# Kernel tuning notes

Hardware: AMD Instinct MI355X
Metric: run time of the kernel (lower is better)

The kernel has to match this reference:

```python
import jax, jax.numpy as jnp
import numpy as np

NUM_ROUNDS = 2
NUM_REVERSE_ROUNDS = 2


def _scatter_mean(x, src, dst, n):
    # PyG mean aggregation: out[i] = mean_{(src->i) in E} x[src]; 0 if no in-edges.
    deg = jax.ops.segment_sum(jnp.ones((src.shape[0],), x.dtype), dst, num_segments=n)
    s = jax.ops.segment_sum(x[src], dst, num_segments=n)
    return s / jnp.maximum(deg, 1.0)[:, None]


def setup_inputs() -> dict:
    key = jax.random.key(0)
    ks = jax.random.split(key, 12)
    N_TEXT, N_NON, E, EMB, R = 100000, 10000, 500000, 256, 500
    N = N_TEXT + N_NON
    PRED_IN = 4 * EMB + 2 * 2 + 2 * 2 * (NUM_ROUNDS + NUM_REVERSE_ROUNDS)  # 1044
    return {
        "h_id_tensor": jax.random.randint(ks[0], (E,), 0, N),
        "r_id_tensor": jax.random.randint(ks[1], (E,), 0, R),
        "t_id_tensor": jax.random.randint(ks[2], (E,), 0, N),
        "q_emb": jax.random.normal(ks[3], (EMB,), jnp.float32),
        "entity_embs": jax.random.normal(ks[4], (N_TEXT, EMB), jnp.float32),
        "num_non_text_entities": N_NON,
        "relation_embs": jax.random.normal(ks[5], (R, EMB), jnp.float32),
        "topic_entity_one_hot": jax.random.uniform(ks[6], (N, 2), jnp.float32),
        "non_text_emb": jax.random.normal(ks[7], (1, EMB), jnp.float32),
        "W1": jax.random.normal(ks[8], (PRED_IN, EMB), jnp.float32) * 0.02,
        "b1": jnp.zeros((EMB,), jnp.float32),
        "W2": jax.random.normal(ks[9], (EMB, 1), jnp.float32) * 0.02,
        "b2": jnp.zeros((1,), jnp.float32),
    }


def reference(h_id_tensor, r_id_tensor, t_id_tensor, q_emb, entity_embs,
              num_non_text_entities, relation_embs, topic_entity_one_hot,
              non_text_emb, W1, b1, W2, b2):
    n = entity_embs.shape[0] + num_non_text_entities
    # h_e base: text entity embs + broadcast non-text embedding
    h_e0 = jnp.concatenate(
        [entity_embs, jnp.broadcast_to(non_text_emb, (num_non_text_entities, non_text_emb.shape[1]))],
        axis=0)
    h_e_list = [h_e0, topic_entity_one_hot]
    # DDE forward rounds: messages flow h_id -> t_id
    h_pe = topic_entity_one_hot
    for _ in range(NUM_ROUNDS):
        h_pe = _scatter_mean(h_pe, h_id_tensor, t_id_tensor, n)
        h_e_list.append(h_pe)
    # reverse rounds: messages flow t_id -> h_id
    h_pe = topic_entity_one_hot
    for _ in range(NUM_REVERSE_ROUNDS):
        h_pe = _scatter_mean(h_pe, t_id_tensor, h_id_tensor, n)
        h_e_list.append(h_pe)
    h_e = jnp.concatenate(h_e_list, axis=1)  # [N, emb + 2 + 2*(R+Rr)]
    e = h_id_tensor.shape[0]
    h_triple = jnp.concatenate(
        [jnp.broadcast_to(q_emb[None, :], (e, q_emb.shape[0])),
         h_e[h_id_tensor],
         relation_embs[r_id_tensor],
         h_e[t_id_tensor]], axis=1)  # [E, 1044]
    hidden = jax.nn.relu(h_triple @ W1 + b1)
    return hidden @ W2 + b2
```

## Files before the change

kernel.cpp:

```cpp
#include <hip/hip_runtime.h>
#include <stdint.h>

#define EMB 256
#define LDKB 288
#define DDE 10

typedef __attribute__((ext_vector_type(8))) short short8;
typedef __attribute__((ext_vector_type(4))) float f32x4;

__device__ __forceinline__ unsigned short f2bf(float f) {
    union { float f; unsigned int u; } v; v.f = f;
    unsigned int u = v.u;
    unsigned int r = (u + 0x7FFFu + ((u >> 16) & 1u)) >> 16;
    return (unsigned short)r;
}
__device__ __forceinline__ float bf2f(unsigned short b) {
    union { unsigned int u; float f; } v; v.u = ((unsigned int)b) << 16;
    return v.f;
}

#define FPSCALE 1048576.0f
#define FPINV   (1.0f / 1048576.0f)

__device__ __forceinline__ unsigned long long pack2(float a, float b) {
    unsigned int ua = (unsigned int)(a * FPSCALE);
    unsigned int ub = (unsigned int)(b * FPSCALE);
    return ((unsigned long long)ua << 36) | ((unsigned long long)ub << 10);
}
__device__ __forceinline__ float2 unpack2(unsigned long long v) {
    float d = fmaxf((float)(unsigned int)(v & 0x3FFULL), 1.0f);
    return make_float2((float)((v >> 36) & 0x3FFFFFFULL) * FPINV / d,
                       (float)((v >> 10) & 0x3FFFFFFULL) * FPINV / d);
}
__device__ __forceinline__ float2 unpack2d(unsigned long long v, float d) {
    return make_float2((float)((v >> 36) & 0x3FFFFFFULL) * FPINV / d,
                       (float)((v >> 10) & 0x3FFFFFFULL) * FPINV / d);
}


__global__ void k_r1_fused(const int* __restrict__ h_id, const int* __restrict__ t_id,
                           const float2* __restrict__ topic,
                           unsigned long long* __restrict__ fwd,
                           unsigned long long* __restrict__ rev, int E, int SC1, int COPY, int WT_BLK,
                           int TOTAL,
                           const float4* __restrict__ entity, const float4* __restrict__ nontext,
                           ushort4* __restrict__ he4, int n_text, int N,
                           const float* __restrict__ W1, unsigned short* __restrict__ wT,
                           const float* __restrict__ qv, const float* __restrict__ rel,
                           const float* __restrict__ b1, unsigned short* __restrict__ Prb) {
    const int b = blockIdx.x;
    const int sc_before = (int)(((long long)b * SC1) / TOTAL);
    const int is_scatter = (int)(((long long)(b + 1) * SC1) / TOTAL) != sc_before;
    if (is_scatter) {
        int e = sc_before * 256 + threadIdx.x;
        if (e >= E) return;
        int h = h_id[e], t = t_id[e];
        float2 th = topic[h];
        float2 tt = topic[t];
        atomicAdd(&fwd[t], pack2(th.x, th.y) | 1ULL);
        atomicAdd(&rev[h], pack2(tt.x, tt.y) | 1ULL);
        return;
    }
    const int o = b - sc_before;
    if (o < COPY) {
        int idx = o * 256 + threadIdx.x;
        int n = idx >> 6, q = idx & 63;
        float4 v = make_float4(0.f, 0.f, 0.f, 0.f);
        if (n < N) v = (n < n_text) ? entity[(size_t)n * 64 + q] : nontext[q];
        he4[(size_t)n * 64 + q] = make_ushort4(f2bf(v.x), f2bf(v.y), f2bf(v.z), f2bf(v.w));
    } else if (o < COPY + WT_BLK) {
        int idx = (o - COPY) * 256 + threadIdx.x;
        int j = idx / LDKB;
        int k = idx - j * LDKB;
        int col   = (j < EMB) ? j : (j - EMB);
        int baseE = (j < EMB) ? 256 : 778;
        int baseD = (j < EMB) ? 512 : 1034;
        float v = 0.0f;
        if (k < EMB)            v = W1[(long long)(baseE + k) * EMB + col];
        else if (k < EMB + DDE) v = W1[(long long)(baseD + (k - EMB)) * EMB + col];
        wT[idx] = f2bf(v);
    } else {
        int r = o - COPY - WT_BLK;
        int j = threadIdx.x;
        float acc = b1[j];
        for (int k = 0; k < EMB; ++k)
            acc = fmaf(qv[k], W1[(long long)k * EMB + j], acc);
        const float* relr = rel + (long long)r * EMB;
        for (int k = 0; k < EMB; ++k)
            acc = fmaf(relr[k], W1[(long long)(522 + k) * EMB + j], acc);
        Prb[(long long)r * EMB + j] = f2bf(acc);
    }
}


__global__ void k_r2(const int* __restrict__ h_id, const int* __restrict__ t_id,
                     const unsigned long long* __restrict__ fwd,
                     const unsigned long long* __restrict__ rev,
                     unsigned long long* __restrict__ s2,
                     unsigned long long* __restrict__ sr2, int E) {
    int e = blockIdx.x * blockDim.x + threadIdx.x;
    if (e >= E) return;
    int h = h_id[e], t = t_id[e];
    float2 dh = unpack2(fwd[h]);
    float2 rt = unpack2(rev[t]);
    atomicAdd(&s2[t], pack2(dh.x, dh.y));
    atomicAdd(&sr2[h], pack2(rt.x, rt.y));
}

__global__ __launch_bounds__(512) void k_gemm(const unsigned short* __restrict__ he,
                                              const unsigned short* __restrict__ wT,
                                              unsigned short* __restrict__ Ph,
                                              unsigned short* __restrict__ Pt,
                                              const float2* __restrict__ topic,
                                              const unsigned long long* __restrict__ fwd,
                                              const unsigned long long* __restrict__ rev,
                                              const unsigned long long* __restrict__ s2,
                                              const unsigned long long* __restrict__ sr2,
                                              int N) {
    __shared__ __align__(16) unsigned short lA[2][128 * 32];
    __shared__ __align__(16) unsigned short lB[2][256 * 32];
    const int t = threadIdx.x;
    const int lane = t & 63;
    const int w = t >> 6;
    const int bswz = (blockIdx.x & 7) * ((int)gridDim.x >> 3) + (blockIdx.x >> 3);
    const int br = bswz >> 1;
    const int bc = bswz & 1;
    const int wr = w >> 2;
    const int wc = w & 3;

    f32x4 acc[4][4];
#pragma unroll
    for (int r = 0; r < 4; ++r)
#pragma unroll
        for (int c = 0; c < 4; ++c)
            acc[r][c] = (f32x4){0.f, 0.f, 0.f, 0.f};

    const char* baseA = (const char*)he + (size_t)(br * 128) * (EMB * 2);
    const char* baseB = (const char*)wT + (size_t)(bc * 256) * (LDKB * 2);

    const int rowX = t >> 2;
    const int colb = (t & 3) * 16;

    auto stage = [&](int k0, int buf) {
        if (k0 < EMB) {
            const char* srcA = baseA + (size_t)rowX * (EMB * 2) + k0 * 2 + colb;
            __builtin_amdgcn_global_load_lds((const __attribute__((address_space(1))) void*)srcA,
                                             (__attribute__((address_space(3))) void*)((char*)lA[buf] + t * 16), 16, 0, 0);
        } else {
            const int n = br * 128 + rowX;
            short8 hv = (short8){0, 0, 0, 0, 0, 0, 0, 0};
            const int q4 = t & 3;
            if (n < N) {
                if (q4 == 0) {
                    float2 tp = topic[n];
                    unsigned long long f = fwd[n];
                    unsigned long long r = rev[n];
                    float df = fmaxf((float)(unsigned int)(f & 0x3FFULL), 1.0f);
                    float2 d1 = unpack2d(f, df);
                    float2 d2 = unpack2d(s2[n], df);
                    float2 r1 = unpack2(r);
                    hv[0] = (short)f2bf(tp.x); hv[1] = (short)f2bf(tp.y);
                    hv[2] = (short)f2bf(d1.x); hv[3] = (short)f2bf(d1.y);
                    hv[4] = (short)f2bf(d2.x); hv[5] = (short)f2bf(d2.y);
                    hv[6] = (short)f2bf(r1.x); hv[7] = (short)f2bf(r1.y);
                } else if (q4 == 1) {
                    unsigned long long r = rev[n];
                    float dr = fmaxf((float)(unsigned int)(r & 0x3FFULL), 1.0f);
                    float2 r2 = unpack2d(sr2[n], dr);
                    hv[0] = (short)f2bf(r2.x); hv[1] = (short)f2bf(r2.y);
                }
            }
            *(short8*)((char*)lA[buf] + rowX * 64 + q4 * 16) = hv;
        }
        const char* srcB0 = baseB + (size_t)rowX * (LDKB * 2) + k0 * 2 + colb;
        const char* srcB1 = baseB + (size_t)(rowX + 128) * (LDKB * 2) + k0 * 2 + colb;
        __builtin_amdgcn_global_load_lds((const __attribute__((address_space(1))) void*)srcB0,
                                         (__attribute__((address_space(3))) void*)((char*)lB[buf] + t * 16), 16, 0, 0);
        __builtin_amdgcn_global_load_lds((const __attribute__((address_space(1))) void*)srcB1,
                                         (__attribute__((address_space(3))) void*)((char*)lB[buf] + 8192 + t * 16), 16, 0, 0);
    };

    const int NK = LDKB / 32;
    stage(0, 0);
    __syncthreads();

    for (int k = 0; k < NK; ++k) {
        const int cur = k & 1;
        if (k + 1 < NK) stage((k + 1) * 32, cur ^ 1);

        short8 af[4], bfr[4];
#pragma unroll
        for (int r = 0; r < 4; ++r) {
            int arow = wr * 64 + r * 16 + (lane & 15);
            af[r] = *(const short8*)(lA[cur] + arow * 32 + (lane >> 4) * 8);
        }
#pragma unroll
        for (int c = 0; c < 4; ++c) {
            int brow = wc * 64 + c * 16 + (lane & 15);
            bfr[c] = *(const short8*)(lB[cur] + brow * 32 + (lane >> 4) * 8);
        }
#pragma unroll
        for (int r = 0; r < 4; ++r)
#pragma unroll
            for (int c = 0; c < 4; ++c)
                acc[r][c] = __builtin_amdgcn_mfma_f32_16x16x32_bf16(af[r], bfr[c], acc[r][c], 0, 0, 0);

        __syncthreads();
    }

    unsigned short* Pout = bc ? Pt : Ph;
    const int nbase = wc * 64;
    const int mbase = br * 128 + wr * 64 + (lane >> 4) * 4;
#pragma unroll
    for (int r = 0; r < 4; ++r) {
#pragma unroll
        for (int c = 0; c < 4; ++c) {
            int n = nbase + c * 16 + (lane & 15);
#pragma unroll
            for (int i = 0; i < 4; ++i) {
                int m = mbase + r * 16 + i;
                Pout[(size_t)m * EMB + n] = f2bf(acc[r][c][i]);
            }
        }
    }
}

__global__ __launch_bounds__(256) void k_edge(
    const int* __restrict__ h_id, const int* __restrict__ r_id, const int* __restrict__ t_id,
    const unsigned short* __restrict__ Ph, const unsigned short* __restrict__ Pt,
    const unsigned short* __restrict__ Prb, const float* __restrict__ W2,
    const float* __restrict__ b2, float* __restrict__ out, int E) {
    int lane = threadIdx.x & 63;
    int gw = (blockIdx.x * blockDim.x + threadIdx.x) >> 6;
    int nw = (gridDim.x * blockDim.x) >> 6;
    float4 w2 = *(const float4*)(W2 + 4 * lane);
    float bb = b2[0];
    const int lo = 4 * lane;
    for (int e = gw; e < E; e += nw) {
        int h = h_id[e], r = r_id[e], t = t_id[e];
        ushort4 ph = *(const ushort4*)(Ph + (size_t)h * EMB + lo);
        ushort4 pt = *(const ushort4*)(Pt + (size_t)t * EMB + lo);
        ushort4 pr = *(const ushort4*)(Prb + (size_t)r * EMB + lo);
        float v, acc;
        v = bf2f(pr.x) + bf2f(ph.x) + bf2f(pt.x); acc  = fmaxf(v, 0.f) * w2.x;
        v = bf2f(pr.y) + bf2f(ph.y) + bf2f(pt.y); acc += fmaxf(v, 0.f) * w2.y;
        v = bf2f(pr.z) + bf2f(ph.z) + bf2f(pt.z); acc += fmaxf(v, 0.f) * w2.z;
        v = bf2f(pr.w) + bf2f(ph.w) + bf2f(pt.w); acc += fmaxf(v, 0.f) * w2.w;
#pragma unroll
        for (int m = 32; m >= 1; m >>= 1) acc += __shfl_xor(acc, m, 64);
        if (lane == 0) out[e] = acc + bb;
    }
}


extern "C" void kernel_launch(void* const* d_in, const int* in_sizes, int n_in,
                              void* d_out, int out_size, void* d_ws, size_t ws_size,
                              hipStream_t stream) {
    const int*   h_id    = (const int*)d_in[0];
    const int*   r_id    = (const int*)d_in[1];
    const int*   t_id    = (const int*)d_in[2];
    const float* q       = (const float*)d_in[3];
    const float* entity  = (const float*)d_in[4];
    const float* rel     = (const float*)d_in[6];
    const float* topic   = (const float*)d_in[7];
    const float* nontext = (const float*)d_in[8];
    const float* W1      = (const float*)d_in[9];
    const float* b1      = (const float*)d_in[10];
    const float* W2      = (const float*)d_in[11];
    const float* b2      = (const float*)d_in[12];

    const int E      = in_sizes[0];
    const int n_text = in_sizes[4] / EMB;
    const int N      = in_sizes[7] / 2;
    const int R      = in_sizes[6] / EMB;
    const int Mpad   = (N + 127) & ~127;

    char* p = (char*)d_ws;
    auto alloc = [&](size_t bytes) {
        char* r = p;
        p += (bytes + 255) & ~(size_t)255;
        return r;
    };
    unsigned long long* fwd = (unsigned long long*)alloc((size_t)Mpad * 8);
    unsigned long long* rev = (unsigned long long*)alloc((size_t)Mpad * 8);
    unsigned long long* s2  = (unsigned long long*)alloc((size_t)Mpad * 8);
    unsigned long long* sr2 = (unsigned long long*)alloc((size_t)Mpad * 8);
    size_t zero_bytes = (size_t)(p - (char*)d_ws);
    unsigned short* he  = (unsigned short*)alloc((size_t)Mpad * EMB * 2);
    unsigned short* wT  = (unsigned short*)alloc((size_t)512 * LDKB * 2);
    unsigned short* Prb = (unsigned short*)alloc((size_t)R * EMB * 2);
    unsigned short* Ph  = (unsigned short*)alloc((size_t)Mpad * EMB * 2);
    unsigned short* Pt  = (unsigned short*)alloc((size_t)Mpad * EMB * 2);

    hipMemsetAsync(d_ws, 0, zero_bytes, stream);

    const int T = 256;
    const int SC1 = (E + T - 1) / T;
    const int COPY = Mpad / 4;
    const int WT_BLK = (512 * LDKB) / T;
    const int TOTAL = SC1 + COPY + WT_BLK + R;

    k_r1_fused<<<TOTAL, T, 0, stream>>>(
        h_id, t_id, (const float2*)topic, fwd, rev, E, SC1, COPY, WT_BLK, TOTAL,
        (const float4*)entity, (const float4*)nontext, (ushort4*)he, n_text, N,
        W1, wT, q, rel, b1, Prb);
    k_r2<<<SC1, T, 0, stream>>>(h_id, t_id, fwd, rev, s2, sr2, E);

    k_gemm<<<(Mpad / 128) * 2, 512, 0, stream>>>(he, wT, Ph, Pt,
                                                 (const float2*)topic, fwd, rev, s2, sr2, N);

    k_edge<<<4096, T, 0, stream>>>(h_id, r_id, t_id, Ph, Pt, Prb, W2, b2, (float*)d_out, E);
}
```

Measured before the change: 296.2 us.

## Overlap second DDE scatter round with node GEMM by moving round-2 terms to edge kernel

The second-round scatter (s2/sr2) no longer runs as its own kernel before the GEMM. Its blocks are interleaved into the GEMM launch, and the GEMM A-tile now carries only the topic, round-1 and reverse round-1 features. The round-2 contributions are instead packed per node by a small k_pack kernel and applied in the edge kernel through a per-column coefficient table (cw) taken from W1. The aim is to drop a dependent launch and run atomics alongside the matrix work, at the cost of an extra pack kernel, an extra 8-byte gather per edge endpoint, and 16 more FMAs per lane per edge.

```diff
diff --git a/kernel.cpp b/kernel.cpp
--- a/kernel.cpp
+++ b/kernel.cpp
@@ -42,12 +42,13 @@
                            const float2* __restrict__ topic,
                            unsigned long long* __restrict__ fwd,
                            unsigned long long* __restrict__ rev, int E, int SC1, int COPY, int WT_BLK,
-                           int TOTAL,
+                           int R, int TOTAL,
                            const float4* __restrict__ entity, const float4* __restrict__ nontext,
                            ushort4* __restrict__ he4, int n_text, int N,
                            const float* __restrict__ W1, unsigned short* __restrict__ wT,
                            const float* __restrict__ qv, const float* __restrict__ rel,
-                           const float* __restrict__ b1, unsigned short* __restrict__ Prb) {
+                           const float* __restrict__ b1, unsigned short* __restrict__ Prb,
+                           float* __restrict__ cw) {
     const int b = blockIdx.x;
     const int sc_before = (int)(((long long)b * SC1) / TOTAL);
     const int is_scatter = (int)(((long long)(b + 1) * SC1) / TOTAL) != sc_before;
@@ -79,7 +80,7 @@
         if (k < EMB)            v = W1[(long long)(baseE + k) * EMB + col];
         else if (k < EMB + DDE) v = W1[(long long)(baseD + (k - EMB)) * EMB + col];
         wT[idx] = f2bf(v);
-    } else {
+    } else if (o < COPY + WT_BLK + R) {
         int r = o - COPY - WT_BLK;
         int j = threadIdx.x;
         float acc = b1[j];
@@ -89,40 +90,51 @@
         for (int k = 0; k < EMB; ++k)
             acc = fmaf(relr[k], W1[(long long)(522 + k) * EMB + j], acc);
         Prb[(long long)r * EMB + j] = f2bf(acc);
-    }
-}
-
-
-__global__ void k_r2(const int* __restrict__ h_id, const int* __restrict__ t_id,
-                     const unsigned long long* __restrict__ fwd,
-                     const unsigned long long* __restrict__ rev,
-                     unsigned long long* __restrict__ s2,
-                     unsigned long long* __restrict__ sr2, int E) {
-    int e = blockIdx.x * blockDim.x + threadIdx.x;
-    if (e >= E) return;
-    int h = h_id[e], t = t_id[e];
-    float2 dh = unpack2(fwd[h]);
-    float2 rt = unpack2(rev[t]);
-    atomicAdd(&s2[t], pack2(dh.x, dh.y));
-    atomicAdd(&sr2[h], pack2(rt.x, rt.y));
-}
-
-__global__ __launch_bounds__(512) void k_gemm(const unsigned short* __restrict__ he,
-                                              const unsigned short* __restrict__ wT,
-                                              unsigned short* __restrict__ Ph,
-                                              unsigned short* __restrict__ Pt,
-                                              const float2* __restrict__ topic,
-                                              const unsigned long long* __restrict__ fwd,
-                                              const unsigned long long* __restrict__ rev,
-                                              const unsigned long long* __restrict__ s2,
-                                              const unsigned long long* __restrict__ sr2,
-                                              int N) {
+    } else {
+        int idx = (o - COPY - WT_BLK - R) * 256 + threadIdx.x;
+        if (idx < 2048) {
+            int j = idx >> 2, c = idx & 3;
+            int col   = (j < EMB) ? j : (j - EMB);
+            int baseD = (j < EMB) ? 512 : 1034;
+            int row   = baseD + ((c < 2) ? (4 + c) : (8 + (c - 2)));
+            cw[idx] = W1[(long long)row * EMB + col];
+        }
+    }
+}
+
+__global__ __launch_bounds__(512) void k_gemm_r2(const unsigned short* __restrict__ he,
+                                                 const unsigned short* __restrict__ wT,
+                                                 unsigned short* __restrict__ Ph,
+                                                 unsigned short* __restrict__ Pt,
+                                                 const float2* __restrict__ topic,
+                                                 const unsigned long long* __restrict__ fwd,
+                                                 const unsigned long long* __restrict__ rev,
+                                                 unsigned long long* __restrict__ s2,
+                                                 unsigned long long* __restrict__ sr2,
+                                                 const int* __restrict__ h_id,
+                                                 const int* __restrict__ t_id,
+                                                 int N, int E, int GB, int TOTAL) {
     __shared__ __align__(16) unsigned short lA[2][128 * 32];
     __shared__ __align__(16) unsigned short lB[2][256 * 32];
+    const int b = blockIdx.x;
+    const int g_before = (int)(((long long)b * GB) / TOTAL);
+    const int is_gemm = (int)(((long long)(b + 1) * GB) / TOTAL) != g_before;
+    if (!is_gemm) {
+        int e = (b - g_before) * 512 + threadIdx.x;
+        if (e < E) {
+            int h = h_id[e], t = t_id[e];
+            float2 dh = unpack2(fwd[h]);
+            float2 rt = unpack2(rev[t]);
+            atomicAdd(&s2[t], pack2(dh.x, dh.y));
+            atomicAdd(&sr2[h], pack2(rt.x, rt.y));
+        }
+        return;
+    }
     const int t = threadIdx.x;
     const int lane = t & 63;
     const int w = t >> 6;
-    const int bswz = (blockIdx.x & 7) * ((int)gridDim.x >> 3) + (blockIdx.x >> 3);
+    const int o = g_before;
+    const int bswz = (o & 7) * (GB >> 3) + (o >> 3);
     const int br = bswz >> 1;
     const int bc = bswz & 1;
     const int wr = w >> 2;
@@ -150,25 +162,15 @@
             const int n = br * 128 + rowX;
             short8 hv = (short8){0, 0, 0, 0, 0, 0, 0, 0};
             const int q4 = t & 3;
-            if (n < N) {
-                if (q4 == 0) {
-                    float2 tp = topic[n];
-                    unsigned long long f = fwd[n];
-                    unsigned long long r = rev[n];
-                    float df = fmaxf((float)(unsigned int)(f & 0x3FFULL), 1.0f);
-                    float2 d1 = unpack2d(f, df);
-                    float2 d2 = unpack2d(s2[n], df);
-                    float2 r1 = unpack2(r);
-                    hv[0] = (short)f2bf(tp.x); hv[1] = (short)f2bf(tp.y);
-                    hv[2] = (short)f2bf(d1.x); hv[3] = (short)f2bf(d1.y);
-                    hv[4] = (short)f2bf(d2.x); hv[5] = (short)f2bf(d2.y);
-                    hv[6] = (short)f2bf(r1.x); hv[7] = (short)f2bf(r1.y);
-                } else if (q4 == 1) {
-                    unsigned long long r = rev[n];
-                    float dr = fmaxf((float)(unsigned int)(r & 0x3FFULL), 1.0f);
-                    float2 r2 = unpack2d(sr2[n], dr);
-                    hv[0] = (short)f2bf(r2.x); hv[1] = (short)f2bf(r2.y);
-                }
+            if (n < N && q4 == 0) {
+                float2 tp = topic[n];
+                unsigned long long f = fwd[n];
+                unsigned long long r = rev[n];
+                float2 d1 = unpack2(f);
+                float2 r1 = unpack2(r);
+                hv[0] = (short)f2bf(tp.x); hv[1] = (short)f2bf(tp.y);
+                hv[2] = (short)f2bf(d1.x); hv[3] = (short)f2bf(d1.y);
+                hv[6] = (short)f2bf(r1.x); hv[7] = (short)f2bf(r1.y);
             }
             *(short8*)((char*)lA[buf] + rowX * 64 + q4 * 16) = hv;
         }
@@ -225,27 +227,61 @@
     }
 }
 
+__global__ void k_pack(const unsigned long long* __restrict__ fwd,
+                       const unsigned long long* __restrict__ rev,
+                       const unsigned long long* __restrict__ s2,
+                       const unsigned long long* __restrict__ sr2,
+                       ushort4* __restrict__ dr2, int N, int Mpad) {
+    int n = blockIdx.x * blockDim.x + threadIdx.x;
+    if (n >= Mpad) return;
+    ushort4 v = make_ushort4(0, 0, 0, 0);
+    if (n < N) {
+        float df = fmaxf((float)(unsigned int)(fwd[n] & 0x3FFULL), 1.0f);
+        float dr = fmaxf((float)(unsigned int)(rev[n] & 0x3FFULL), 1.0f);
+        float2 d2 = unpack2d(s2[n], df);
+        float2 r2 = unpack2d(sr2[n], dr);
+        v = make_ushort4(f2bf(d2.x), f2bf(d2.y), f2bf(r2.x), f2bf(r2.y));
+    }
+    dr2[n] = v;
+}
+
 __global__ __launch_bounds__(256) void k_edge(
     const int* __restrict__ h_id, const int* __restrict__ r_id, const int* __restrict__ t_id,
     const unsigned short* __restrict__ Ph, const unsigned short* __restrict__ Pt,
-    const unsigned short* __restrict__ Prb, const float* __restrict__ W2,
+    const unsigned short* __restrict__ Prb, const ushort4* __restrict__ dr2,
+    const float4* __restrict__ cw, const float* __restrict__ W2,
     const float* __restrict__ b2, float* __restrict__ out, int E) {
     int lane = threadIdx.x & 63;
     int gw = (blockIdx.x * blockDim.x + threadIdx.x) >> 6;
     int nw = (gridDim.x * blockDim.x) >> 6;
-    float4 w2 = *(const float4*)(W2 + 4 * lane);
+    const int lo = 4 * lane;
+    float w2c[4];
+    *(float4*)w2c = *(const float4*)(W2 + lo);
     float bb = b2[0];
-    const int lo = 4 * lane;
+    float4 cH[4], cT[4];
+#pragma unroll
+    for (int c = 0; c < 4; ++c) { cH[c] = cw[lo + c]; cT[c] = cw[256 + lo + c]; }
+
     for (int e = gw; e < E; e += nw) {
         int h = h_id[e], r = r_id[e], t = t_id[e];
         ushort4 ph = *(const ushort4*)(Ph + (size_t)h * EMB + lo);
         ushort4 pt = *(const ushort4*)(Pt + (size_t)t * EMB + lo);
         ushort4 pr = *(const ushort4*)(Prb + (size_t)r * EMB + lo);
-        float v, acc;
-        v = bf2f(pr.x) + bf2f(ph.x) + bf2f(pt.x); acc  = fmaxf(v, 0.f) * w2.x;
-        v = bf2f(pr.y) + bf2f(ph.y) + bf2f(pt.y); acc += fmaxf(v, 0.f) * w2.y;
-        v = bf2f(pr.z) + bf2f(ph.z) + bf2f(pt.z); acc += fmaxf(v, 0.f) * w2.z;
-        v = bf2f(pr.w) + bf2f(ph.w) + bf2f(pt.w); acc += fmaxf(v, 0.f) * w2.w;
+        ushort4 dh = dr2[h];
+        ushort4 dt = dr2[t];
+        float d2hx = bf2f(dh.x), d2hy = bf2f(dh.y), r2hx = bf2f(dh.z), r2hy = bf2f(dh.w);
+        float d2tx = bf2f(dt.x), d2ty = bf2f(dt.y), r2tx = bf2f(dt.z), r2ty = bf2f(dt.w);
+        const unsigned short* phs = (const unsigned short*)&ph;
+        const unsigned short* pts = (const unsigned short*)&pt;
+        const unsigned short* prs = (const unsigned short*)&pr;
+        float acc = 0.f;
+#pragma unroll
+        for (int c = 0; c < 4; ++c) {
+            float v = bf2f(prs[c]) + bf2f(phs[c]) + bf2f(pts[c]);
+            v += d2hx * cH[c].x + d2hy * cH[c].y + r2hx * cH[c].z + r2hy * cH[c].w;
+            v += d2tx * cT[c].x + d2ty * cT[c].y + r2tx * cT[c].z + r2ty * cT[c].w;
+            acc += fmaxf(v, 0.f) * w2c[c];
+        }
 #pragma unroll
         for (int m = 32; m >= 1; m >>= 1) acc += __shfl_xor(acc, m, 64);
         if (lane == 0) out[e] = acc + bb;
@@ -291,6 +327,8 @@
     unsigned short* Prb = (unsigned short*)alloc((size_t)R * EMB * 2);
     unsigned short* Ph  = (unsigned short*)alloc((size_t)Mpad * EMB * 2);
     unsigned short* Pt  = (unsigned short*)alloc((size_t)Mpad * EMB * 2);
+    ushort4*        dr2 = (ushort4*)alloc((size_t)Mpad * 8);
+    float*          cw  = (float*)alloc((size_t)512 * 4 * 4);
 
     hipMemsetAsync(d_ws, 0, zero_bytes, stream);
 
@@ -298,16 +336,22 @@
     const int SC1 = (E + T - 1) / T;
     const int COPY = Mpad / 4;
     const int WT_BLK = (512 * LDKB) / T;
-    const int TOTAL = SC1 + COPY + WT_BLK + R;
-
-    k_r1_fused<<<TOTAL, T, 0, stream>>>(
-        h_id, t_id, (const float2*)topic, fwd, rev, E, SC1, COPY, WT_BLK, TOTAL,
+    const int COEF = 8;
+    const int TOTAL1 = SC1 + COPY + WT_BLK + R + COEF;
+
+    k_r1_fused<<<TOTAL1, T, 0, stream>>>(
+        h_id, t_id, (const float2*)topic, fwd, rev, E, SC1, COPY, WT_BLK, R, TOTAL1,
         (const float4*)entity, (const float4*)nontext, (ushort4*)he, n_text, N,
-        W1, wT, q, rel, b1, Prb);
-    k_r2<<<SC1, T, 0, stream>>>(h_id, t_id, fwd, rev, s2, sr2, E);
-
-    k_gemm<<<(Mpad / 128) * 2, 512, 0, stream>>>(he, wT, Ph, Pt,
-                                                 (const float2*)topic, fwd, rev, s2, sr2, N);
-
-    k_edge<<<4096, T, 0, stream>>>(h_id, r_id, t_id, Ph, Pt, Prb, W2, b2, (float*)d_out, E);
-}
+        W1, wT, q, rel, b1, Prb, cw);
+
+    const int GB  = (Mpad / 128) * 2;
+    const int R2B = (E + 511) / 512;
+    k_gemm_r2<<<GB + R2B, 512, 0, stream>>>(he, wT, Ph, Pt,
+                                            (const float2*)topic, fwd, rev, s2, sr2,
+                                            h_id, t_id, N, E, GB, GB + R2B);
+
+    k_pack<<<(Mpad + T - 1) / T, T, 0, stream>>>(fwd, rev, s2, sr2, dr2, N, Mpad);
+
+    k_edge<<<4096, T, 0, stream>>>(h_id, r_id, t_id, Ph, Pt, Prb, dr2,
+                                   (const float4*)cw, W2, b2, (float*)d_out, E);
+}
```

Result: no change. 294.1 us (-0.7%).

## Merge both scatter rounds into one kernel with a global completion flag

Applied to the files above, without the earlier changes.

Folds the second scatter-mean round into the first fused kernel. Round-2 blocks spin on a global counter until every round-1 scatter block has finished, and scatter and copy blocks are interleaved so independent copy work fills the gaps. This removes one kernel launch and its boundary, and lets the copy, weight-transpose and relation-projection work overlap with both scatter phases. The risk is a deadlock if the waiting blocks occupy all slots before the round-1 blocks are scheduled, which the code relies on dispatch order to avoid. It also adds spin-wait overhead and fences.

```diff
diff --git a/kernel.cpp b/kernel.cpp
--- a/kernel.cpp
+++ b/kernel.cpp
@@ -38,73 +38,100 @@
 }
 
 
-__global__ void k_r1_fused(const int* __restrict__ h_id, const int* __restrict__ t_id,
-                           const float2* __restrict__ topic,
-                           unsigned long long* __restrict__ fwd,
-                           unsigned long long* __restrict__ rev, int E, int SC1, int COPY, int WT_BLK,
-                           int TOTAL,
-                           const float4* __restrict__ entity, const float4* __restrict__ nontext,
-                           ushort4* __restrict__ he4, int n_text, int N,
-                           const float* __restrict__ W1, unsigned short* __restrict__ wT,
-                           const float* __restrict__ qv, const float* __restrict__ rel,
-                           const float* __restrict__ b1, unsigned short* __restrict__ Prb) {
+__global__ __launch_bounds__(256, 8) void k_mega(
+    const int* __restrict__ h_id, const int* __restrict__ t_id,
+    const float2* __restrict__ topic,
+    unsigned long long* __restrict__ fwd, unsigned long long* __restrict__ rev,
+    unsigned long long* __restrict__ s2, unsigned long long* __restrict__ sr2,
+    unsigned long long* __restrict__ flag,
+    int E, int SC1, int R2B, int COPY_C, int WT_BLK,
+    const float4* __restrict__ entity, const float4* __restrict__ nontext,
+    ushort4* __restrict__ he4, int n_text, int N,
+    const float* __restrict__ W1, unsigned short* __restrict__ wT,
+    const float* __restrict__ qv, const float* __restrict__ rel,
+    const float* __restrict__ b1, unsigned short* __restrict__ Prb) {
     const int b = blockIdx.x;
-    const int sc_before = (int)(((long long)b * SC1) / TOTAL);
-    const int is_scatter = (int)(((long long)(b + 1) * SC1) / TOTAL) != sc_before;
-    if (is_scatter) {
-        int e = sc_before * 256 + threadIdx.x;
-        if (e >= E) return;
-        int h = h_id[e], t = t_id[e];
-        float2 th = topic[h];
-        float2 tt = topic[t];
-        atomicAdd(&fwd[t], pack2(th.x, th.y) | 1ULL);
-        atomicAdd(&rev[h], pack2(tt.x, tt.y) | 1ULL);
-        return;
+    const int A = 2 * SC1, B = 2 * R2B;
+    int copyIdx;
+    if (b < A) {
+        if (!(b & 1)) {
+            int e = (b >> 1) * 256 + threadIdx.x;
+            if (e < E) {
+                int h = h_id[e], t = t_id[e];
+                float2 th = topic[h];
+                float2 tt = topic[t];
+                unsigned long long o1 = atomicAdd(&fwd[t], pack2(th.x, th.y) | 1ULL);
+                unsigned long long o2 = atomicAdd(&rev[h], pack2(tt.x, tt.y) | 1ULL);
+                asm volatile("" :: "v"(o1), "v"(o2));
+            }
+            __threadfence();
+            __syncthreads();
+            if (threadIdx.x == 0) atomicAdd(flag, 1ULL);
+            return;
+        }
+        copyIdx = b >> 1;
+    } else if (b < A + B) {
+        const int q = b - A;
+        if (!(q & 1)) {
+            const int blk = q >> 1;
+            if (threadIdx.x == 0) {
+                while (__hip_atomic_load(flag, __ATOMIC_ACQUIRE, __HIP_MEMORY_SCOPE_AGENT)
+                       < (unsigned long long)SC1)
+                    __builtin_amdgcn_s_sleep(16);
+            }
+            __syncthreads();
+#pragma unroll
+            for (int it = 0; it < 2; ++it) {
+                int e = blk * 512 + it * 256 + threadIdx.x;
+                if (e < E) {
+                    int h = h_id[e], t = t_id[e];
+                    unsigned long long f = __hip_atomic_load(&fwd[h], __ATOMIC_RELAXED,
+                                                             __HIP_MEMORY_SCOPE_AGENT);
+                    unsigned long long r = __hip_atomic_load(&rev[t], __ATOMIC_RELAXED,
+                                                             __HIP_MEMORY_SCOPE_AGENT);
+                    float2 dh = unpack2(f);
+                    float2 rt = unpack2(r);
+                    atomicAdd(&s2[t], pack2(dh.x, dh.y));
+                    atomicAdd(&sr2[h], pack2(rt.x, rt.y));
+                }
+            }
+            return;
+        }
+        copyIdx = SC1 + (q >> 1);
+    } else {
+        const int q = b - A - B;
+        if (q < COPY_C) {
+            copyIdx = SC1 + R2B + q;
+        } else if (q < COPY_C + WT_BLK) {
+            int idx = (q - COPY_C) * 256 + threadIdx.x;
+            int j = idx / LDKB;
+            int k = idx - j * LDKB;
+            int col   = (j < EMB) ? j : (j - EMB);
+            int baseE = (j < EMB) ? 256 : 778;
+            int baseD = (j < EMB) ? 512 : 1034;
+            float v = 0.0f;
+            if (k < EMB)            v = W1[(long long)(baseE + k) * EMB + col];
+            else if (k < EMB + DDE) v = W1[(long long)(baseD + (k - EMB)) * EMB + col];
+            wT[idx] = f2bf(v);
+            return;
+        } else {
+            int r = q - COPY_C - WT_BLK;
+            int j = threadIdx.x;
+            float acc = b1[j];
+            for (int k = 0; k < EMB; ++k)
+                acc = fmaf(qv[k], W1[(long long)k * EMB + j], acc);
+            const float* relr = rel + (long long)r * EMB;
+            for (int k = 0; k < EMB; ++k)
+                acc = fmaf(relr[k], W1[(long long)(522 + k) * EMB + j], acc);
+            Prb[(long long)r * EMB + j] = f2bf(acc);
+            return;
+        }
     }
-    const int o = b - sc_before;
-    if (o < COPY) {
-        int idx = o * 256 + threadIdx.x;
-        int n = idx >> 6, q = idx & 63;
-        float4 v = make_float4(0.f, 0.f, 0.f, 0.f);
-        if (n < N) v = (n < n_text) ? entity[(size_t)n * 64 + q] : nontext[q];
-        he4[(size_t)n * 64 + q] = make_ushort4(f2bf(v.x), f2bf(v.y), f2bf(v.z), f2bf(v.w));
-    } else if (o < COPY + WT_BLK) {
-        int idx = (o - COPY) * 256 + threadIdx.x;
-        int j = idx / LDKB;
-        int k = idx - j * LDKB;
-        int col   = (j < EMB) ? j : (j - EMB);
-        int baseE = (j < EMB) ? 256 : 778;
-        int baseD = (j < EMB) ? 512 : 1034;
-        float v = 0.0f;
-        if (k < EMB)            v = W1[(long long)(baseE + k) * EMB + col];
-        else if (k < EMB + DDE) v = W1[(long long)(baseD + (k - EMB)) * EMB + col];
-        wT[idx] = f2bf(v);
-    } else {
-        int r = o - COPY - WT_BLK;
-        int j = threadIdx.x;
-        float acc = b1[j];
-        for (int k = 0; k < EMB; ++k)
-            acc = fmaf(qv[k], W1[(long long)k * EMB + j], acc);
-        const float* relr = rel + (long long)r * EMB;
-        for (int k = 0; k < EMB; ++k)
-            acc = fmaf(relr[k], W1[(long long)(522 + k) * EMB + j], acc);
-        Prb[(long long)r * EMB + j] = f2bf(acc);
-    }
-}
-
-
-__global__ void k_r2(const int* __restrict__ h_id, const int* __restrict__ t_id,
-                     const unsigned long long* __restrict__ fwd,
-                     const unsigned long long* __restrict__ rev,
-                     unsigned long long* __restrict__ s2,
-                     unsigned long long* __restrict__ sr2, int E) {
-    int e = blockIdx.x * blockDim.x + threadIdx.x;
-    if (e >= E) return;
-    int h = h_id[e], t = t_id[e];
-    float2 dh = unpack2(fwd[h]);
-    float2 rt = unpack2(rev[t]);
-    atomicAdd(&s2[t], pack2(dh.x, dh.y));
-    atomicAdd(&sr2[h], pack2(rt.x, rt.y));
+    int idx = copyIdx * 256 + threadIdx.x;
+    int n = idx >> 6, qq = idx & 63;
+    float4 v = make_float4(0.f, 0.f, 0.f, 0.f);
+    if (n < N) v = (n < n_text) ? entity[(size_t)n * 64 + qq] : nontext[qq];
+    he4[(size_t)n * 64 + qq] = make_ushort4(f2bf(v.x), f2bf(v.y), f2bf(v.z), f2bf(v.w));
 }
 
 __global__ __launch_bounds__(512) void k_gemm(const unsigned short* __restrict__ he,
@@ -281,10 +308,11 @@
         p += (bytes + 255) & ~(size_t)255;
         return r;
     };
-    unsigned long long* fwd = (unsigned long long*)alloc((size_t)Mpad * 8);
-    unsigned long long* rev = (unsigned long long*)alloc((size_t)Mpad * 8);
-    unsigned long long* s2  = (unsigned long long*)alloc((size_t)Mpad * 8);
-    unsigned long long* sr2 = (unsigned long long*)alloc((size_t)Mpad * 8);
+    unsigned long long* fwd  = (unsigned long long*)alloc((size_t)Mpad * 8);
+    unsigned long long* rev  = (unsigned long long*)alloc((size_t)Mpad * 8);
+    unsigned long long* s2   = (unsigned long long*)alloc((size_t)Mpad * 8);
+    unsigned long long* sr2  = (unsigned long long*)alloc((size_t)Mpad * 8);
+    unsigned long long* flag = (unsigned long long*)alloc(256);
     size_t zero_bytes = (size_t)(p - (char*)d_ws);
     unsigned short* he  = (unsigned short*)alloc((size_t)Mpad * EMB * 2);
     unsigned short* wT  = (unsigned short*)alloc((size_t)512 * LDKB * 2);
@@ -295,16 +323,18 @@
     hipMemsetAsync(d_ws, 0, zero_bytes, stream);
 
     const int T = 256;
-    const int SC1 = (E + T - 1) / T;
-    const int COPY = Mpad / 4;
+    const int SC1    = (E + T - 1) / T;
+    const int R2B    = (E + 511) / 512;
+    const int COPY   = Mpad / 4;
+    const int COPY_C = COPY - SC1 - R2B;
     const int WT_BLK = (512 * LDKB) / T;
-    const int TOTAL = SC1 + COPY + WT_BLK + R;
-
-    k_r1_fused<<<TOTAL, T, 0, stream>>>(
-        h_id, t_id, (const float2*)topic, fwd, rev, E, SC1, COPY, WT_BLK, TOTAL,
+    const int TOTAL  = 2 * SC1 + 2 * R2B + COPY_C + WT_BLK + R;
+
+    k_mega<<<TOTAL, T, 0, stream>>>(
+        h_id, t_id, (const float2*)topic, fwd, rev, s2, sr2, flag,
+        E, SC1, R2B, COPY_C, WT_BLK,
         (const float4*)entity, (const float4*)nontext, (ushort4*)he, n_text, N,
         W1, wT, q, rel, b1, Prb);
-    k_r2<<<SC1, T, 0, stream>>>(h_id, t_id, fwd, rev, s2, sr2, E);
 
     k_gemm<<<(Mpad / 128) * 2, 512, 0, stream>>>(he, wT, Ph, Pt,
                                                  (const float2*)topic, fwd, rev, s2, sr2, N);
```

New measurement: 671.3 us. +126.7%, slower.

## Split independent copy and prep work across both scatter rounds to balance kernels

Applied to the files above, without the earlier changes.

Moves part of the embedding-to-bf16 copy, plus all the W1 transpose and relation-projection work, out of the first scatter kernel and into the second. Each scatter round now runs alongside independent work, where before the second round ran alone. The split ratio between the two kernels is hardcoded. It aims to overlap latency-bound atomic scatters with bandwidth-bound copies, at the cost of a fixed ratio that may not balance well.

```diff
diff --git a/kernel.cpp b/kernel.cpp
--- a/kernel.cpp
+++ b/kernel.cpp
@@ -37,12 +37,48 @@
                        (float)((v >> 10) & 0x3FFFFFFULL) * FPINV / d);
 }
 
+__device__ __forceinline__ void he_copy_role(int copyIdx, int tid,
+                                             const float4* __restrict__ entity,
+                                             const float4* __restrict__ nontext,
+                                             ushort4* __restrict__ he4,
+                                             int n_text, int N) {
+    int idx = copyIdx * 256 + tid;
+    int n = idx >> 6, q = idx & 63;
+    float4 v = make_float4(0.f, 0.f, 0.f, 0.f);
+    if (n < N) v = (n < n_text) ? entity[(size_t)n * 64 + q] : nontext[q];
+    he4[(size_t)n * 64 + q] = make_ushort4(f2bf(v.x), f2bf(v.y), f2bf(v.z), f2bf(v.w));
+}
+
 
 __global__ void k_r1_fused(const int* __restrict__ h_id, const int* __restrict__ t_id,
                            const float2* __restrict__ topic,
                            unsigned long long* __restrict__ fwd,
-                           unsigned long long* __restrict__ rev, int E, int SC1, int COPY, int WT_BLK,
-                           int TOTAL,
+                           unsigned long long* __restrict__ rev, int E, int SC1, int TOTAL,
+                           const float4* __restrict__ entity, const float4* __restrict__ nontext,
+                           ushort4* __restrict__ he4, int n_text, int N) {
+    const int b = blockIdx.x;
+    const int sc_before = (int)(((long long)b * SC1) / TOTAL);
+    const int is_scatter = (int)(((long long)(b + 1) * SC1) / TOTAL) != sc_before;
+    if (is_scatter) {
+        int e = sc_before * 256 + threadIdx.x;
+        if (e >= E) return;
+        int h = h_id[e], t = t_id[e];
+        float2 th = topic[h];
+        float2 tt = topic[t];
+        atomicAdd(&fwd[t], pack2(th.x, th.y) | 1ULL);
+        atomicAdd(&rev[h], pack2(tt.x, tt.y) | 1ULL);
+        return;
+    }
+    he_copy_role(b - sc_before, threadIdx.x, entity, nontext, he4, n_text, N);
+}
+
+
+__global__ void k_r2_fused(const int* __restrict__ h_id, const int* __restrict__ t_id,
+                           const unsigned long long* __restrict__ fwd,
+                           const unsigned long long* __restrict__ rev,
+                           unsigned long long* __restrict__ s2,
+                           unsigned long long* __restrict__ sr2,
+                           int E, int SC1, int C1, int C2, int WT_BLK, int TOTAL,
                            const float4* __restrict__ entity, const float4* __restrict__ nontext,
                            ushort4* __restrict__ he4, int n_text, int N,
                            const float* __restrict__ W1, unsigned short* __restrict__ wT,
@@ -55,21 +91,17 @@
         int e = sc_before * 256 + threadIdx.x;
         if (e >= E) return;
         int h = h_id[e], t = t_id[e];
-        float2 th = topic[h];
-        float2 tt = topic[t];
-        atomicAdd(&fwd[t], pack2(th.x, th.y) | 1ULL);
-        atomicAdd(&rev[h], pack2(tt.x, tt.y) | 1ULL);
+        float2 dh = unpack2(fwd[h]);
+        float2 rt = unpack2(rev[t]);
+        atomicAdd(&s2[t], pack2(dh.x, dh.y));
+        atomicAdd(&sr2[h], pack2(rt.x, rt.y));
         return;
     }
     const int o = b - sc_before;
-    if (o < COPY) {
-        int idx = o * 256 + threadIdx.x;
-        int n = idx >> 6, q = idx & 63;
-        float4 v = make_float4(0.f, 0.f, 0.f, 0.f);
-        if (n < N) v = (n < n_text) ? entity[(size_t)n * 64 + q] : nontext[q];
-        he4[(size_t)n * 64 + q] = make_ushort4(f2bf(v.x), f2bf(v.y), f2bf(v.z), f2bf(v.w));
-    } else if (o < COPY + WT_BLK) {
-        int idx = (o - COPY) * 256 + threadIdx.x;
+    if (o < C2) {
+        he_copy_role(C1 + o, threadIdx.x, entity, nontext, he4, n_text, N);
+    } else if (o < C2 + WT_BLK) {
+        int idx = (o - C2) * 256 + threadIdx.x;
         int j = idx / LDKB;
         int k = idx - j * LDKB;
         int col   = (j < EMB) ? j : (j - EMB);
@@ -80,7 +112,7 @@
         else if (k < EMB + DDE) v = W1[(long long)(baseD + (k - EMB)) * EMB + col];
         wT[idx] = f2bf(v);
     } else {
-        int r = o - COPY - WT_BLK;
+        int r = o - C2 - WT_BLK;
         int j = threadIdx.x;
         float acc = b1[j];
         for (int k = 0; k < EMB; ++k)
@@ -90,21 +122,6 @@
             acc = fmaf(relr[k], W1[(long long)(522 + k) * EMB + j], acc);
         Prb[(long long)r * EMB + j] = f2bf(acc);
     }
-}
-
-
-__global__ void k_r2(const int* __restrict__ h_id, const int* __restrict__ t_id,
-                     const unsigned long long* __restrict__ fwd,
-                     const unsigned long long* __restrict__ rev,
-                     unsigned long long* __restrict__ s2,
-                     unsigned long long* __restrict__ sr2, int E) {
-    int e = blockIdx.x * blockDim.x + threadIdx.x;
-    if (e >= E) return;
-    int h = h_id[e], t = t_id[e];
-    float2 dh = unpack2(fwd[h]);
-    float2 rt = unpack2(rev[t]);
-    atomicAdd(&s2[t], pack2(dh.x, dh.y));
-    atomicAdd(&sr2[h], pack2(rt.x, rt.y));
 }
 
 __global__ __launch_bounds__(512) void k_gemm(const unsigned short* __restrict__ he,
@@ -295,16 +312,22 @@
     hipMemsetAsync(d_ws, 0, zero_bytes, stream);
 
     const int T = 256;
-    const int SC1 = (E + T - 1) / T;
-    const int COPY = Mpad / 4;
+    const int SC1    = (E + T - 1) / T;
+    const int COPY   = Mpad / 4;
+    const int C1     = (COPY * 44) / 100;
+    const int C2     = COPY - C1;
     const int WT_BLK = (512 * LDKB) / T;
-    const int TOTAL = SC1 + COPY + WT_BLK + R;
-
-    k_r1_fused<<<TOTAL, T, 0, stream>>>(
-        h_id, t_id, (const float2*)topic, fwd, rev, E, SC1, COPY, WT_BLK, TOTAL,
+    const int TOT1   = SC1 + C1;
+    const int TOT2   = SC1 + C2 + WT_BLK + R;
+
+    k_r1_fused<<<TOT1, T, 0, stream>>>(
+        h_id, t_id, (const float2*)topic, fwd, rev, E, SC1, TOT1,
+        (const float4*)entity, (const float4*)nontext, (ushort4*)he, n_text, N);
+
+    k_r2_fused<<<TOT2, T, 0, stream>>>(
+        h_id, t_id, fwd, rev, s2, sr2, E, SC1, C1, C2, WT_BLK, TOT2,
         (const float4*)entity, (const float4*)nontext, (ushort4*)he, n_text, N,
         W1, wT, q, rel, b1, Prb);
-    k_r2<<<SC1, T, 0, stream>>>(h_id, t_id, fwd, rev, s2, sr2, E);
 
     k_gemm<<<(Mpad / 128) * 2, 512, 0, stream>>>(he, wT, Ph, Pt,
                                                  (const float2*)topic, fwd, rev, s2, sr2, N);
```

Result: no change. 300.3 us (+1.4%).
